# Performance work log

Hardware: AMD Instinct MI355X
Metric: run time of the kernel (lower is better)

The kernel has to match this reference:

```python
import jax, jax.numpy as jnp
import numpy as np

EPS = 0.5  # diffusion epsilon from init_kwargs

def setup_inputs() -> dict:
    key = jax.random.key(0)
    k = jax.random.split(key, 7)
    B, N0, N1, n = 1024, 32, 32, 64
    Mu0 = jax.random.normal(k[0], (N0, n), dtype=jnp.float32) * 2.0
    Mu1 = jax.random.normal(k[1], (N1, n), dtype=jnp.float32) * 2.0
    # diagonal covariances must be positive
    S0 = jax.random.uniform(k[2], (N0, n), dtype=jnp.float32, minval=0.1, maxval=1.0)
    S1 = jax.random.uniform(k[3], (N1, n), dtype=jnp.float32, minval=0.1, maxval=1.0)
    Lam = jax.random.uniform(k[4], (N0, N1), dtype=jnp.float32, minval=0.0, maxval=1.0)
    Lam = Lam / Lam.sum()  # transport plan sums to 1
    X = jax.random.normal(k[5], (B, n), dtype=jnp.float32)
    t = jnp.float32(0.3)
    return {"X": X, "Mu0": Mu0, "Mu1": Mu1, "S0": S0, "S1": S1, "Lam": Lam, "t": t}

def reference(X, Mu0, Mu1, S0, S1, Lam, t):
    eps2 = EPS * EPS
    S0e = S0[:, None, :]        # (N0,1,n)
    S1e = S1[None, :, :]        # (1,N1,n)
    Ds = jnp.sqrt(4.0 * S0e * S1e + EPS ** 4)
    Cs = 0.5 * (Ds - eps2)                       # (N0,N1,n)
    mu_t = (1.0 - t) * Mu0[:, None, :] + t * Mu1[None, :, :]  # (N0,N1,n)
    Sigma = (1.0 - t) ** 2 * S0e + t ** 2 * S1e + 2.0 * t * (1.0 - t) * (Cs + 0.5 * eps2)
    # St = Pt - Qt - eps^2 * t
    St = t * S1e + (1.0 - t) * Cs - ((1.0 - t) * S0e + t * Cs) - eps2 * t
    K = St / Sigma                               # (N0,N1,n)
    v = Mu1[None, :, :] - Mu0[:, None, :]        # (N0,N1,n)
    d = X[:, None, None, :] - mu_t               # (B,N0,N1,n)
    U = K * d + v                                # (B,N0,N1,n)
    # diag-Normal log_prob plus n/2*log(2pi) == -0.5*sum(d^2/Sigma + log Sigma)
    logw = -0.5 * jnp.sum(d * d / Sigma + jnp.log(Sigma), axis=-1)  # (B,N0,N1)
    W = jnp.exp(jnp.clip(logw, -50.0, 50.0)) * Lam                  # (B,N0,N1)
    num = jnp.einsum('bijn,bij->bn', U, W)       # (B,n)
    den = jnp.sum(W, axis=(1, 2))[:, None]       # (B,1)
    return num / den
```

## Files before the change

kernel.cpp:

```cpp
#include <hip/hip_runtime.h>
#include <math.h>

#define EPS2f 0.25f
#define EPS4f 0.0625f

__device__ __forceinline__ float rl(float v, int l) {
    return __int_as_float(__builtin_amdgcn_readlane(__float_as_int(v), l));
}

__global__ __launch_bounds__(256) void precomp_kernel(
    const float* __restrict__ Mu0, const float* __restrict__ Mu1,
    const float* __restrict__ S0,  const float* __restrict__ S1,
    const float* __restrict__ tptr,
    float2* __restrict__ AB2, float2* __restrict__ KV2,
    float* __restrict__ C0)
{
    __shared__ float2 abS[4][67];
    __shared__ float2 kvS[4][64];

    const int tid = threadIdx.x;
    const int k   = tid & 63;
    const int ijl = tid >> 6;
    const int ij0 = blockIdx.x << 2;
    const int ij  = ij0 + ijl;
    const int i   = ij >> 5;
    const int j   = ij & 31;
    const float t   = *tptr;
    const float omt = 1.0f - t;

    const float s0 = S0[i * 64 + k];
    const float s1 = S1[j * 64 + k];
    const float m0 = Mu0[i * 64 + k];
    const float m1 = Mu1[j * 64 + k];

    const float ds  = sqrtf(4.0f * s0 * s1 + EPS4f);
    const float cs  = 0.5f * (ds - EPS2f);
    const float mt  = omt * m0 + t * m1;
    const float sig = omt * omt * s0 + t * t * s1
                    + 2.0f * t * omt * (cs + 0.5f * EPS2f);
    const float isig = 1.0f / sig;
    const float st = t * s1 - omt * s0 + (omt - t) * cs - EPS2f * t;
    const float kk = st * isig;
    const float v  = m1 - m0;

    abS[ijl][k] = make_float2(isig, 2.0f * mt * isig);
    kvS[ijl][k] = make_float2(kk, v - kk * mt);

    float c = mt * mt * isig + __logf(sig);
    #pragma unroll
    for (int off = 32; off >= 1; off >>= 1)
        c += __shfl_xor(c, off, 64);
    if (k == 0) C0[ij] = c;

    __syncthreads();

    {
        const int k2   = tid >> 3;
        const int ijl2 = (tid >> 1) & 3;
        const int par  = tid & 1;
        AB2[(k2 << 11) + ((ij0 + ijl2) << 1) + par] = abS[ijl2][2 * k2 + par];
    }
    {
        const int pr  = tid >> 7;
        const int k6  = (tid >> 1) & 63;
        const int par = tid & 1;
        KV2[(blockIdx.x << 8) + tid] = kvS[(pr << 1) + par][k6];
    }
}

__global__ __launch_bounds__(1024) void gmm_main_kernel(
    const float* __restrict__ X,   const float* __restrict__ Lam,
    const float* __restrict__ C0,
    const float4* __restrict__ AB4, const float4* __restrict__ KV4,
    float* __restrict__ out)
{
    __shared__ float red[16 * 64 * 5];
    __shared__ float denp[16 * 4];

    const int tid  = threadIdx.x;
    const int lane = tid & 63;
    const int w    = tid >> 6;
    const int b0   = blockIdx.x << 2;

    const float xk0 = X[(b0 + 0) * 64 + lane];
    const float xk1 = X[(b0 + 1) * 64 + lane];
    const float xk2 = X[(b0 + 2) * 64 + lane];
    const float xk3 = X[(b0 + 3) * 64 + lane];

    const int ij = tid;
    const float4* __restrict__ abp = AB4 + ij;
    const float c0 = C0[ij];
    const float lm = Lam[ij];

    float4 ab[8];
    #pragma unroll
    for (int g = 0; g < 8; ++g) ab[g] = abp[g << 10];

    float qa = 0.f, qb = 0.f, qc = 0.f, qd = 0.f;
    #pragma unroll
    for (int k2 = 0; k2 < 32; ++k2) {
        const float4 a = ab[k2 & 7];
        if (k2 + 8 < 32) ab[k2 & 7] = abp[(k2 + 8) << 10];
        const float xe0 = rl(xk0, 2 * k2),     xo0 = rl(xk0, 2 * k2 + 1);
        const float xe1 = rl(xk1, 2 * k2),     xo1 = rl(xk1, 2 * k2 + 1);
        const float xe2 = rl(xk2, 2 * k2),     xo2 = rl(xk2, 2 * k2 + 1);
        const float xe3 = rl(xk3, 2 * k2),     xo3 = rl(xk3, 2 * k2 + 1);
        qa = fmaf(fmaf(a.x, xe0, -a.y), xe0, qa);
        qb = fmaf(fmaf(a.x, xe1, -a.y), xe1, qb);
        qc = fmaf(fmaf(a.x, xe2, -a.y), xe2, qc);
        qd = fmaf(fmaf(a.x, xe3, -a.y), xe3, qd);
        qa = fmaf(fmaf(a.z, xo0, -a.w), xo0, qa);
        qb = fmaf(fmaf(a.z, xo1, -a.w), xo1, qb);
        qc = fmaf(fmaf(a.z, xo2, -a.w), xo2, qc);
        qd = fmaf(fmaf(a.z, xo3, -a.w), xo3, qd);
    }

    #define WCALC(q) (__expf(fminf(fmaxf(-0.5f * ((q) + c0), -50.f), 50.f)) * lm)
    float4 wv4;
    wv4.x = WCALC(qa); wv4.y = WCALC(qb); wv4.z = WCALC(qc); wv4.w = WCALC(qd);
    #undef WCALC

    const int p0 = w << 5;
    float4 kvb[8];
    #pragma unroll
    for (int q = 0; q < 8; ++q) kvb[q] = KV4[((p0 + q) << 6) + lane];

    float d0 = wv4.x, d1 = wv4.y, d2 = wv4.z, d3 = wv4.w;
    #pragma unroll
    for (int off = 32; off >= 1; off >>= 1) {
        d0 += __shfl_xor(d0, off, 64);
        d1 += __shfl_xor(d1, off, 64);
        d2 += __shfl_xor(d2, off, 64);
        d3 += __shfl_xor(d3, off, 64);
    }
    if (lane == 0) {
        denp[w * 4 + 0] = d0; denp[w * 4 + 1] = d1;
        denp[w * 4 + 2] = d2; denp[w * 4 + 3] = d3;
    }

    float n0 = 0.f, n1 = 0.f, n2 = 0.f, n3 = 0.f;
    #pragma unroll
    for (int p = 0; p < 32; ++p) {
        const float4 kv = kvb[p & 7];
        if (p + 8 < 32) kvb[p & 7] = KV4[((p0 + p + 8) << 6) + lane];
        const float wex = rl(wv4.x, 2 * p),     wox = rl(wv4.x, 2 * p + 1);
        const float wey = rl(wv4.y, 2 * p),     woy = rl(wv4.y, 2 * p + 1);
        const float wez = rl(wv4.z, 2 * p),     woz = rl(wv4.z, 2 * p + 1);
        const float wew = rl(wv4.w, 2 * p),     wow = rl(wv4.w, 2 * p + 1);
        float u;
        u = fmaf(kv.x, xk0, kv.y); n0 = fmaf(wex, u, n0);
        u = fmaf(kv.x, xk1, kv.y); n1 = fmaf(wey, u, n1);
        u = fmaf(kv.x, xk2, kv.y); n2 = fmaf(wez, u, n2);
        u = fmaf(kv.x, xk3, kv.y); n3 = fmaf(wew, u, n3);
        u = fmaf(kv.z, xk0, kv.w); n0 = fmaf(wox, u, n0);
        u = fmaf(kv.z, xk1, kv.w); n1 = fmaf(woy, u, n1);
        u = fmaf(kv.z, xk2, kv.w); n2 = fmaf(woz, u, n2);
        u = fmaf(kv.z, xk3, kv.w); n3 = fmaf(wow, u, n3);
    }
    {
        float* r = &red[(w * 64 + lane) * 5];
        r[0] = n0; r[1] = n1; r[2] = n2; r[3] = n3;
    }
    __syncthreads();

    if (tid < 256) {
        const int bb = tid >> 6, k = tid & 63;
        float s = 0.f, d = 0.f;
        #pragma unroll
        for (int ww = 0; ww < 16; ++ww) {
            s += red[(ww * 64 + k) * 5 + bb];
            d += denp[ww * 4 + bb];
        }
        out[(b0 + bb) * 64 + k] = s / d;
    }
}

extern "C" void kernel_launch(void* const* d_in, const int* in_sizes, int n_in,
                              void* d_out, int out_size, void* d_ws, size_t ws_size,
                              hipStream_t stream) {
    const float* X   = (const float*)d_in[0];
    const float* Mu0 = (const float*)d_in[1];
    const float* Mu1 = (const float*)d_in[2];
    const float* S0  = (const float*)d_in[3];
    const float* S1  = (const float*)d_in[4];
    const float* Lam = (const float*)d_in[5];
    const float* t   = (const float*)d_in[6];
    float* out = (float*)d_out;

    char* ws = (char*)d_ws;
    float2* AB2 = (float2*)(ws);
    float2* KV2 = (float2*)(ws + (512 << 10));
    float*  C0  = (float*)(ws + (1024 << 10));

    precomp_kernel<<<256, 256, 0, stream>>>(Mu0, Mu1, S0, S1, t, AB2, KV2, C0);
    gmm_main_kernel<<<256, 1024, 0, stream>>>(X, Lam, C0,
                                              (const float4*)AB2,
                                              (const float4*)KV2, out);
}
```

Before: 80.92 us.

## Split mixture components across blocks with 8 rows per wave and separate combine kernel

```diff
diff --git a/kernel.cpp b/kernel.cpp
--- a/kernel.cpp
+++ b/kernel.cpp
@@ -68,111 +68,106 @@
     }
 }
 
-__global__ __launch_bounds__(1024) void gmm_main_kernel(
+__global__ __launch_bounds__(256) void gmm_main_kernel(
     const float* __restrict__ X,   const float* __restrict__ Lam,
     const float* __restrict__ C0,
     const float4* __restrict__ AB4, const float4* __restrict__ KV4,
-    float* __restrict__ out)
+    float* __restrict__ nump, float* __restrict__ denp)
 {
-    __shared__ float red[16 * 64 * 5];
-    __shared__ float denp[16 * 4];
+    const int tid    = threadIdx.x;
+    const int lane   = tid & 63;
+    const int rowsub = tid >> 6;
+    const int bx     = blockIdx.x;
+    const int c      = bx & 15;
+    const int g      = bx >> 4;
+    const int r0     = (g << 5) + (rowsub << 3);
+    const int ij     = (c << 6) + lane;
 
-    const int tid  = threadIdx.x;
-    const int lane = tid & 63;
-    const int w    = tid >> 6;
-    const int b0   = blockIdx.x << 2;
+    float xr[8];
+    #pragma unroll
+    for (int u = 0; u < 8; ++u) xr[u] = X[(r0 + u) * 64 + lane];
 
-    const float xk0 = X[(b0 + 0) * 64 + lane];
-    const float xk1 = X[(b0 + 1) * 64 + lane];
-    const float xk2 = X[(b0 + 2) * 64 + lane];
-    const float xk3 = X[(b0 + 3) * 64 + lane];
-
-    const int ij = tid;
-    const float4* __restrict__ abp = AB4 + ij;
     const float c0 = C0[ij];
     const float lm = Lam[ij];
 
-    float4 ab[8];
+    const float4* __restrict__ abp = AB4 + ij;
+    float4 ab[4];
     #pragma unroll
-    for (int g = 0; g < 8; ++g) ab[g] = abp[g << 10];
+    for (int pf = 0; pf < 4; ++pf) ab[pf] = abp[pf << 10];
 
-    float qa = 0.f, qb = 0.f, qc = 0.f, qd = 0.f;
+    float q[8] = {0.f, 0.f, 0.f, 0.f, 0.f, 0.f, 0.f, 0.f};
     #pragma unroll
     for (int k2 = 0; k2 < 32; ++k2) {
-        const float4 a = ab[k2 & 7];
-        if (k2 + 8 < 32) ab[k2 & 7] = abp[(k2 + 8) << 10];
-        const float xe0 = rl(xk0, 2 * k2),     xo0 = rl(xk0, 2 * k2 + 1);
-        const float xe1 = rl(xk1, 2 * k2),     xo1 = rl(xk1, 2 * k2 + 1);
-        const float xe2 = rl(xk2, 2 * k2),     xo2 = rl(xk2, 2 * k2 + 1);
-        const float xe3 = rl(xk3, 2 * k2),     xo3 = rl(xk3, 2 * k2 + 1);
-        qa = fmaf(fmaf(a.x, xe0, -a.y), xe0, qa);
-        qb = fmaf(fmaf(a.x, xe1, -a.y), xe1, qb);
-        qc = fmaf(fmaf(a.x, xe2, -a.y), xe2, qc);
-        qd = fmaf(fmaf(a.x, xe3, -a.y), xe3, qd);
-        qa = fmaf(fmaf(a.z, xo0, -a.w), xo0, qa);
-        qb = fmaf(fmaf(a.z, xo1, -a.w), xo1, qb);
-        qc = fmaf(fmaf(a.z, xo2, -a.w), xo2, qc);
-        qd = fmaf(fmaf(a.z, xo3, -a.w), xo3, qd);
+        const float4 a = ab[k2 & 3];
+        if (k2 + 4 < 32) ab[k2 & 3] = abp[(k2 + 4) << 10];
+        #pragma unroll
+        for (int u = 0; u < 8; ++u) {
+            const float xe = rl(xr[u], 2 * k2);
+            const float xo = rl(xr[u], 2 * k2 + 1);
+            q[u] = fmaf(fmaf(a.x, xe, -a.y), xe, q[u]);
+            q[u] = fmaf(fmaf(a.z, xo, -a.w), xo, q[u]);
+        }
     }
 
-    #define WCALC(q) (__expf(fminf(fmaxf(-0.5f * ((q) + c0), -50.f), 50.f)) * lm)
-    float4 wv4;
-    wv4.x = WCALC(qa); wv4.y = WCALC(qb); wv4.z = WCALC(qc); wv4.w = WCALC(qd);
-    #undef WCALC
+    float wv[8];
+    #pragma unroll
+    for (int u = 0; u < 8; ++u)
+        wv[u] = __expf(fminf(fmaxf(-0.5f * (q[u] + c0), -50.f), 50.f)) * lm;
 
-    const int p0 = w << 5;
-    float4 kvb[8];
+    const float4* __restrict__ kvp = KV4 + (c << 11) + lane;
+    float4 kvb[4];
     #pragma unroll
-    for (int q = 0; q < 8; ++q) kvb[q] = KV4[((p0 + q) << 6) + lane];
+    for (int pf = 0; pf < 4; ++pf) kvb[pf] = kvp[pf << 6];
 
-    float d0 = wv4.x, d1 = wv4.y, d2 = wv4.z, d3 = wv4.w;
+    float dsum[8];
+    #pragma unroll
+    for (int u = 0; u < 8; ++u) dsum[u] = wv[u];
     #pragma unroll
     for (int off = 32; off >= 1; off >>= 1) {
-        d0 += __shfl_xor(d0, off, 64);
-        d1 += __shfl_xor(d1, off, 64);
-        d2 += __shfl_xor(d2, off, 64);
-        d3 += __shfl_xor(d3, off, 64);
-    }
-    if (lane == 0) {
-        denp[w * 4 + 0] = d0; denp[w * 4 + 1] = d1;
-        denp[w * 4 + 2] = d2; denp[w * 4 + 3] = d3;
+        #pragma unroll
+        for (int u = 0; u < 8; ++u) dsum[u] += __shfl_xor(dsum[u], off, 64);
     }
 
-    float n0 = 0.f, n1 = 0.f, n2 = 0.f, n3 = 0.f;
+    float nacc[8] = {0.f, 0.f, 0.f, 0.f, 0.f, 0.f, 0.f, 0.f};
     #pragma unroll
     for (int p = 0; p < 32; ++p) {
-        const float4 kv = kvb[p & 7];
-        if (p + 8 < 32) kvb[p & 7] = KV4[((p0 + p + 8) << 6) + lane];
-        const float wex = rl(wv4.x, 2 * p),     wox = rl(wv4.x, 2 * p + 1);
-        const float wey = rl(wv4.y, 2 * p),     woy = rl(wv4.y, 2 * p + 1);
-        const float wez = rl(wv4.z, 2 * p),     woz = rl(wv4.z, 2 * p + 1);
-        const float wew = rl(wv4.w, 2 * p),     wow = rl(wv4.w, 2 * p + 1);
-        float u;
-        u = fmaf(kv.x, xk0, kv.y); n0 = fmaf(wex, u, n0);
-        u = fmaf(kv.x, xk1, kv.y); n1 = fmaf(wey, u, n1);
-        u = fmaf(kv.x, xk2, kv.y); n2 = fmaf(wez, u, n2);
-        u = fmaf(kv.x, xk3, kv.y); n3 = fmaf(wew, u, n3);
-        u = fmaf(kv.z, xk0, kv.w); n0 = fmaf(wox, u, n0);
-        u = fmaf(kv.z, xk1, kv.w); n1 = fmaf(woy, u, n1);
-        u = fmaf(kv.z, xk2, kv.w); n2 = fmaf(woz, u, n2);
-        u = fmaf(kv.z, xk3, kv.w); n3 = fmaf(wow, u, n3);
+        const float4 kv = kvb[p & 3];
+        if (p + 4 < 32) kvb[p & 3] = kvp[(p + 4) << 6];
+        #pragma unroll
+        for (int u = 0; u < 8; ++u) {
+            const float We = rl(wv[u], 2 * p);
+            const float Wo = rl(wv[u], 2 * p + 1);
+            const float ue = fmaf(kv.x, xr[u], kv.y);
+            nacc[u] = fmaf(We, ue, nacc[u]);
+            const float uo = fmaf(kv.z, xr[u], kv.w);
+            nacc[u] = fmaf(Wo, uo, nacc[u]);
+        }
     }
-    {
-        float* r = &red[(w * 64 + lane) * 5];
-        r[0] = n0; r[1] = n1; r[2] = n2; r[3] = n3;
+
+    #pragma unroll
+    for (int u = 0; u < 8; ++u)
+        nump[(c * 1024 + r0 + u) * 64 + lane] = nacc[u];
+
+    float dv = dsum[0];
+    #pragma unroll
+    for (int u = 1; u < 8; ++u) dv = (lane == u) ? dsum[u] : dv;
+    if (lane < 8) denp[(c << 10) + r0 + lane] = dv;
+}
+
+__global__ __launch_bounds__(256) void combine_kernel(
+    const float* __restrict__ nump, const float* __restrict__ denp,
+    float* __restrict__ out)
+{
+    const int idx = blockIdx.x * 256 + threadIdx.x;
+    const int b = idx >> 6;
+    const int k = idx & 63;
+    float s = 0.f, d = 0.f;
+    #pragma unroll
+    for (int c = 0; c < 16; ++c) {
+        s += nump[(c * 1024 + b) * 64 + k];
+        d += denp[(c << 10) + b];
     }
-    __syncthreads();
-
-    if (tid < 256) {
-        const int bb = tid >> 6, k = tid & 63;
-        float s = 0.f, d = 0.f;
-        #pragma unroll
-        for (int ww = 0; ww < 16; ++ww) {
-            s += red[(ww * 64 + k) * 5 + bb];
-            d += denp[ww * 4 + bb];
-        }
-        out[(b0 + bb) * 64 + k] = s / d;
-    }
+    out[idx] = s / d;
 }
 
 extern "C" void kernel_launch(void* const* d_in, const int* in_sizes, int n_in,
@@ -188,12 +183,15 @@
     float* out = (float*)d_out;
 
     char* ws = (char*)d_ws;
-    float2* AB2 = (float2*)(ws);
-    float2* KV2 = (float2*)(ws + (512 << 10));
-    float*  C0  = (float*)(ws + (1024 << 10));
+    float2* AB2  = (float2*)(ws);
+    float2* KV2  = (float2*)(ws + (512 << 10));
+    float*  C0   = (float*)(ws + (1024 << 10));
+    float*  nump = (float*)(ws + (2 << 20));
+    float*  denp = (float*)(ws + (6 << 20));
 
     precomp_kernel<<<256, 256, 0, stream>>>(Mu0, Mu1, S0, S1, t, AB2, KV2, C0);
-    gmm_main_kernel<<<256, 1024, 0, stream>>>(X, Lam, C0,
-                                              (const float4*)AB2,
-                                              (const float4*)KV2, out);
+    gmm_main_kernel<<<512, 256, 0, stream>>>(X, Lam, C0,
+                                             (const float4*)AB2,
+                                             (const float4*)KV2, nump, denp);
+    combine_kernel<<<256, 256, 0, stream>>>(nump, denp, out);
 }
```

Result: slower. 85.81 us (+6.0%).
